# Performance work log

Hardware: AMD Instinct MI355X
Metric: run time of the kernel (lower is better)

The kernel has to match this reference:

```python
import jax, jax.numpy as jnp
import numpy as np
import math

B, E, K, H, NH = 8, 256, 64, 768, 12
HD = H // NH


def setup_inputs() -> dict:
    key = jax.random.key(0)
    ks = jax.random.split(key, 10)
    s = 0.02
    return {
        "q_in": jax.random.normal(ks[0], (B, E, 1, H), jnp.float32),
        "k_in": jax.random.normal(ks[1], (B, E, K, H), jnp.float32),
        "v_in": jax.random.normal(ks[2], (B, E, K, H), jnp.float32),
        "type_score": jax.random.uniform(ks[3], (B, E, 1, 1, K), jnp.float32),
        "Wq": jax.random.normal(ks[4], (H, H), jnp.float32) * s,
        "bq": jnp.zeros((H,), jnp.float32),
        "Wk": jax.random.normal(ks[5], (H, H), jnp.float32) * s,
        "bk": jnp.zeros((H,), jnp.float32),
        "Wv": jax.random.normal(ks[6], (H, H), jnp.float32) * s,
        "bv": jnp.zeros((H,), jnp.float32),
    }


def _heads(x):
    # [B,E,S,H] -> [B,E,nh,S,hd]
    b, e, s, _ = x.shape
    return x.reshape(b, e, s, NH, HD).transpose(0, 1, 3, 2, 4)


def reference(q_in, k_in, v_in, type_score, Wq, bq, Wk, bk, Wv, bv):
    q = _heads(q_in @ Wq.T + bq)   # [B,E,nh,1,hd]
    k = _heads(k_in @ Wk.T + bk)   # [B,E,nh,K,hd]
    v = _heads(v_in @ Wv.T + bv)   # [B,E,nh,K,hd]
    scores = jnp.einsum('behqd,behkd->behqk', q, k) / math.sqrt(HD)
    probs = jax.nn.softmax(scores, axis=-1)
    # post-softmax type reweighting (dropout = identity in eval)
    probs = probs * type_score
    ctx = jnp.einsum('behqk,behkd->behqd', probs, v)   # [B,E,nh,1,hd]
    ctx = ctx.transpose(0, 1, 3, 2, 4).reshape(B, E, 1, H)
    return ctx.squeeze(-2)  # [B,E,H]
```

## Files before the change

kernel.cpp:

```cpp
#include <hip/hip_runtime.h>
#include <stdint.h>

#define Bdim  8
#define Edim  256
#define Kdim  64
#define Hdim  768
#define NHdim 12
#define HDdim 64

typedef __attribute__((ext_vector_type(8))) short short8;
typedef __attribute__((ext_vector_type(4))) float floatx4;
typedef unsigned short ushort_t;
typedef unsigned int u32;

#define GPLANE (2048*768)

__device__ __forceinline__ float bf2f(ushort_t u){
  union { u32 i; float f; } v; v.i = ((u32)u) << 16; return v.f;
}
__device__ __forceinline__ ushort_t f2bf(float f){
  union { float f; u32 i; } v; v.f = f;
  u32 r = v.i + 0x7fffu + ((v.i >> 16) & 1u);
  return (ushort_t)(r >> 16);
}
__device__ __forceinline__ u32 cvtpk(float lo, float hi){
  u32 r;
  asm("v_cvt_pk_bf16_f32 %0, %1, %2" : "=v"(r) : "v"(lo), "v"(hi));
  return r;
}

__device__ __forceinline__ void async_ld16(void* lds, const void* g){
  __builtin_amdgcn_global_load_lds(
      (const __attribute__((address_space(1))) u32*)(uintptr_t)g,
      (__attribute__((address_space(3))) u32*)(u32)(uintptr_t)lds,
      16, 0, 0);
}

__global__ __launch_bounds__(256, 2)
void gemm_proj(const float* __restrict__ A, const ushort_t* __restrict__ W,
               const float* __restrict__ bias, ushort_t* __restrict__ Cout)
{
  __shared__ __align__(16) char smem[34816];
  const int t    = threadIdx.x;
  const int lane = t & 63;
  const int wave = t >> 6;
  const int wm   = wave >> 1, wn = wave & 1;
  const int n0   = blockIdx.x * 128;
  const int m0   = blockIdx.y * 128;

  floatx4 acc[4][4];
#pragma unroll
  for (int i = 0; i < 4; i++)
#pragma unroll
    for (int j = 0; j < 4; j++) acc[i][j] = (floatx4)0.f;

  int am[4], ac[4];
#pragma unroll
  for (int q = 0; q < 4; q++){ int idx = q*256 + t; am[q] = idx >> 3; ac[q] = idx & 7; }

  float4 areg[4];
  const int NT = Hdim / 32;

  char* const smemc = (char*)smem;
  auto Abase = [&](int b){ return smemc + b*16384; };
  auto Wbase = [&](int b){ return smemc + b*16384 + 8192; };

  auto loadA = [&](int kt){
    const float* Ap = A + (size_t)m0*768 + kt*32;
#pragma unroll
    for (int q = 0; q < 4; q++)
      areg[q] = *(const float4*)(Ap + (size_t)am[q]*768 + ac[q]*4);
  };
  auto writeA = [&](int b){
    char* base = Abase(b);
#pragma unroll
    for (int q = 0; q < 4; q++){
      u32 lo = (u32)f2bf(areg[q].x) | ((u32)f2bf(areg[q].y) << 16);
      u32 hi = (u32)f2bf(areg[q].z) | ((u32)f2bf(areg[q].w) << 16);
      int off = am[q]*64 + ((ac[q]*8) ^ ((am[q]&3) << 4));
      u32* p = (u32*)(base + off);
      p[0] = lo; p[1] = hi;
    }
  };
  auto stageW = [&](int kt, int b){
    char* base = Wbase(b);
#pragma unroll
    for (int i = 0; i < 2; i++){
      int s  = i*256 + t;
      int n  = s >> 2, kc = s & 3;
      int kcs = kc ^ (n & 3);
      const ushort_t* g = W + (size_t)(n0 + n)*768 + kt*32 + kcs*8;
      char* ldst = base + (i*256 + wave*64) * 16;
      async_ld16(ldst, g);
    }
  };
  auto compute = [&](int b){
    char* ab = Abase(b);
    char* wb = Wbase(b);
    short8 af[4], bf[4];
#pragma unroll
    for (int mi = 0; mi < 4; mi++){
      int row = wm*64 + mi*16 + (lane & 15);
      int off = row*64 + (((lane >> 4) * 16) ^ ((row & 3) << 4));
      af[mi] = *(const short8*)(ab + off);
    }
#pragma unroll
    for (int ni = 0; ni < 4; ni++){
      int row = wn*64 + ni*16 + (lane & 15);
      int off = row*64 + (((lane >> 4) * 16) ^ ((row & 3) << 4));
      bf[ni] = *(const short8*)(wb + off);
    }
#pragma unroll
    for (int mi = 0; mi < 4; mi++)
#pragma unroll
      for (int ni = 0; ni < 4; ni++)
        acc[mi][ni] = __builtin_amdgcn_mfma_f32_16x16x32_bf16(af[mi], bf[ni], acc[mi][ni], 0, 0, 0);
  };

  int buf = 0;
  loadA(0);
  stageW(0, 0);
  writeA(0);
  asm volatile("s_waitcnt vmcnt(0)" ::: "memory");
  __syncthreads();

  for (int kt = 0; kt < NT; ++kt){
    if (kt + 1 < NT){
      loadA(kt + 1);
      stageW(kt + 1, buf ^ 1);
    }
    compute(buf);
    if (kt + 1 < NT) writeA(buf ^ 1);
    asm volatile("s_waitcnt vmcnt(0)" ::: "memory");
    __syncthreads();
    buf ^= 1;
  }

  float bvv[4];
#pragma unroll
  for (int ni = 0; ni < 4; ni++) bvv[ni] = bias[n0 + wn*64 + ni*16 + (lane & 15)];

  ushort_t* sc = (ushort_t*)smem;
#pragma unroll
  for (int mi = 0; mi < 4; mi++){
    int row0 = wm*64 + mi*16 + ((lane >> 4) << 2);
#pragma unroll
    for (int ni = 0; ni < 4; ni++){
      int col = wn*64 + ni*16 + (lane & 15);
#pragma unroll
      for (int r = 0; r < 4; r++)
        sc[(row0 + r)*136 + col] = f2bf(acc[mi][ni][r] + bvv[ni]);
    }
  }
  __syncthreads();
  int row = t >> 1, seg = t & 1;
  const char* src = smemc + row*272 + seg*128;
  char* dst = (char*)(Cout + (size_t)(m0 + row)*768 + n0 + seg*64);
#pragma unroll
  for (int c = 0; c < 8; c++)
    *(floatx4*)(dst + c*16) = *(const floatx4*)(src + c*16);
}

__global__ __launch_bounds__(256)
void prep(const float* __restrict__ Wq, const float* __restrict__ Wv,
          const float* __restrict__ Wk, ushort_t* __restrict__ Wqb,
          ushort_t* __restrict__ Wvb, ushort_t* __restrict__ WkTb)
{
  __shared__ float tile[32][33];
  const int b = blockIdx.x;
  if (b < 1152){
    const float* src = (b < 576) ? Wq : Wv;
    ushort_t*    dst = (b < 576) ? Wqb : Wvb;
    int bb = (b < 576) ? b : b - 576;
    int i = (bb * 256 + threadIdx.x) * 4;
    float4 v = *(const float4*)(src + i);
    u32* p = (u32*)(dst + i);
    p[0] = (u32)f2bf(v.x) | ((u32)f2bf(v.y) << 16);
    p[1] = (u32)f2bf(v.z) | ((u32)f2bf(v.w) << 16);
  } else {
    int bb = b - 1152;
    int bo = (bb / 24) * 32;
    int bc = (bb % 24) * 32;
    int tx = threadIdx.x & 31, ty = threadIdx.x >> 5;
#pragma unroll
    for (int i = 0; i < 4; i++)
      tile[ty + 8*i][tx] = Wk[(size_t)(bo + ty + 8*i)*768 + bc + tx];
    __syncthreads();
#pragma unroll
    for (int i = 0; i < 4; i++)
      WkTb[(size_t)(bc + ty + 8*i)*768 + bo + tx] = f2bf(tile[tx][ty + 8*i]);
  }
}

__global__ __launch_bounds__(256)
void gemm_g(const ushort_t* __restrict__ qp, const ushort_t* __restrict__ WkT,
            ushort_t* __restrict__ g)
{
  const int h  = blockIdx.z;
  const int n0 = blockIdx.x * 128;
  const int m0 = blockIdx.y * 128;
  const int t = threadIdx.x, lane = t & 63, wave = t >> 6;
  const int wm = wave >> 1, wn = wave & 1;
  const int hl = lane & 15, jr = lane >> 4;

  floatx4 acc[4][4];
#pragma unroll
  for (int i = 0; i < 4; i++)
#pragma unroll
    for (int j = 0; j < 4; j++) acc[i][j] = (floatx4)0.f;

#pragma unroll
  for (int kt = 0; kt < 2; kt++){
    short8 af[4], bf[4];
#pragma unroll
    for (int mi = 0; mi < 4; mi++)
      af[mi] = *(const short8*)(qp + (size_t)(m0 + wm*64 + mi*16 + hl)*768 + h*64 + kt*32 + jr*8);
#pragma unroll
    for (int ni = 0; ni < 4; ni++)
      bf[ni] = *(const short8*)(WkT + (size_t)(n0 + wn*64 + ni*16 + hl)*768 + h*64 + kt*32 + jr*8);
#pragma unroll
    for (int mi = 0; mi < 4; mi++)
#pragma unroll
      for (int ni = 0; ni < 4; ni++)
        acc[mi][ni] = __builtin_amdgcn_mfma_f32_16x16x32_bf16(af[mi], bf[ni], acc[mi][ni], 0, 0, 0);
  }

  ushort_t* gp = g + (size_t)h * GPLANE;
#pragma unroll
  for (int mi = 0; mi < 4; mi++){
#pragma unroll
    for (int ni = 0; ni < 4; ni++){
      int col = n0 + wn*64 + ni*16 + hl;
#pragma unroll
      for (int r = 0; r < 4; r++){
        int row = m0 + wm*64 + mi*16 + jr*4 + r;
        gp[(size_t)row*768 + col] = f2bf(acc[mi][ni][r]);
      }
    }
  }
}

__global__ __launch_bounds__(384)
void attn_main(const float* __restrict__ k_in, const float* __restrict__ v_in,
               const float* __restrict__ tsc, const ushort_t* __restrict__ g,
               ushort_t* __restrict__ Ug, float* __restrict__ ps_g)
{
  const int be = blockIdx.x;
  const int t = threadIdx.x, lane = t & 63, w = t >> 6;
  const int hl = lane & 15, jr = lane >> 4;

  __shared__ float P[12][64];
  __shared__ float redmax[4][16];
  __shared__ float redsum[4][16];

  float s[4], e[4], gm;
  if (w < 4){
    const float* krow = k_in + (size_t)be*Kdim*768 + (size_t)(w*16 + hl)*768;
    const int hq = (hl < 12) ? hl : 0;
    const ushort_t* grow = g + (size_t)hq*GPLANE + (size_t)be*768;

    floatx4 acc = (floatx4)0.f;
#pragma unroll 4
    for (int kt = 0; kt < 24; kt++){
      int c0 = kt*32 + jr*8;
      float4 f0 = *(const float4*)(krow + c0);
      float4 f1 = *(const float4*)(krow + c0 + 4);
      union { short8 s8; u32 wd[4]; } A;
      A.wd[0] = cvtpk(f0.x, f0.y);
      A.wd[1] = cvtpk(f0.z, f0.w);
      A.wd[2] = cvtpk(f1.x, f1.y);
      A.wd[3] = cvtpk(f1.z, f1.w);
      short8 bf = *(const short8*)(grow + c0);
      acc = __builtin_amdgcn_mfma_f32_16x16x32_bf16(A.s8, bf, acc, 0, 0, 0);
    }
#pragma unroll
    for (int r = 0; r < 4; r++) s[r] = acc[r] * 0.125f;

    float wmax = fmaxf(fmaxf(s[0], s[1]), fmaxf(s[2], s[3]));
    wmax = fmaxf(wmax, __shfl_xor(wmax, 16));
    wmax = fmaxf(wmax, __shfl_xor(wmax, 32));
    if (jr == 0) redmax[w][hl] = wmax;
  }
  __syncthreads();
  if (w < 4){
    gm = fmaxf(fmaxf(redmax[0][hl], redmax[1][hl]),
               fmaxf(redmax[2][hl], redmax[3][hl]));
    float es = 0.f;
#pragma unroll
    for (int r = 0; r < 4; r++){ e[r] = __expf(s[r] - gm); es += e[r]; }
    es += __shfl_xor(es, 16);
    es += __shfl_xor(es, 32);
    if (jr == 0) redsum[w][hl] = es;
  }
  __syncthreads();
  if (w < 4 && hl < 12){
    float S = redsum[0][hl] + redsum[1][hl] + redsum[2][hl] + redsum[3][hl];
    float invS = 1.0f / S;
    float4 t4 = *(const float4*)(tsc + be*64 + w*16 + jr*4);
    float4 pv = make_float4(e[0]*invS*t4.x, e[1]*invS*t4.y,
                            e[2]*invS*t4.z, e[3]*invS*t4.w);
    *(float4*)&P[hl][w*16 + jr*4] = pv;
  }
  __syncthreads();

  if (t < 12){
    float sum = 0.f;
#pragma unroll
    for (int jb = 0; jb < 16; jb++){
      float4 p4 = *(const float4*)&P[t][jb*4];
      sum += p4.x + p4.y + p4.z + p4.w;
    }
    ps_g[be*12 + t] = sum;
  }

  const float* vbase = v_in + (size_t)be*Kdim*768 + 2*t;
  float u0[12], u1[12];
#pragma unroll
  for (int h = 0; h < 12; h++){ u0[h] = 0.f; u1[h] = 0.f; }

  for (int jb = 0; jb < 16; jb++){
    float2 v[4];
#pragma unroll
    for (int q = 0; q < 4; q++)
      v[q] = *(const float2*)(vbase + (size_t)(jb*4 + q)*768);
#pragma unroll
    for (int h = 0; h < 12; h++){
      float4 p4 = *(const float4*)&P[h][jb*4];
      u0[h] += p4.x*v[0].x + p4.y*v[1].x + p4.z*v[2].x + p4.w*v[3].x;
      u1[h] += p4.x*v[0].y + p4.y*v[1].y + p4.z*v[2].y + p4.w*v[3].y;
    }
  }

#pragma unroll
  for (int h = 0; h < 12; h++)
    ((u32*)(Ug + (size_t)h*GPLANE + (size_t)be*768))[t] = cvtpk(u0[h], u1[h]);
}

__global__ __launch_bounds__(256)
void out_proj(const ushort_t* __restrict__ Ug, const ushort_t* __restrict__ Wvb,
              const float* __restrict__ bv, const float* __restrict__ ps_g,
              float* __restrict__ out)
{
  const int h  = blockIdx.y;
  const int m0 = blockIdx.x * 128;
  const int t = threadIdx.x, lane = t & 63, wave = t >> 6;
  const int wm = wave >> 1, wn = wave & 1;
  const int hl = lane & 15, jr = lane >> 4;

  const ushort_t* Up = Ug + (size_t)h*GPLANE;

  floatx4 acc[4][2];
#pragma unroll
  for (int i = 0; i < 4; i++){ acc[i][0] = (floatx4)0.f; acc[i][1] = (floatx4)0.f; }

#pragma unroll 4
  for (int kt = 0; kt < 24; kt++){
    short8 af[4], bf[2];
#pragma unroll
    for (int mi = 0; mi < 4; mi++)
      af[mi] = *(const short8*)(Up + (size_t)(m0 + wm*64 + mi*16 + hl)*768 + kt*32 + jr*8);
#pragma unroll
    for (int ni = 0; ni < 2; ni++)
      bf[ni] = *(const short8*)(Wvb + (size_t)(h*64 + wn*32 + ni*16 + hl)*768 + kt*32 + jr*8);
#pragma unroll
    for (int mi = 0; mi < 4; mi++)
#pragma unroll
      for (int ni = 0; ni < 2; ni++)
        acc[mi][ni] = __builtin_amdgcn_mfma_f32_16x16x32_bf16(af[mi], bf[ni], acc[mi][ni], 0, 0, 0);
  }

  float bvo[2];
#pragma unroll
  for (int ni = 0; ni < 2; ni++) bvo[ni] = bv[h*64 + wn*32 + ni*16 + hl];

#pragma unroll
  for (int mi = 0; mi < 4; mi++){
#pragma unroll
    for (int r = 0; r < 4; r++){
      int be = m0 + wm*64 + mi*16 + jr*4 + r;
      float psv = ps_g[be*12 + h];
#pragma unroll
      for (int ni = 0; ni < 2; ni++)
        out[(size_t)be*768 + h*64 + wn*32 + ni*16 + hl] = acc[mi][ni][r] + bvo[ni]*psv;
    }
  }
}

extern "C" void kernel_launch(void* const* d_in, const int* in_sizes, int n_in,
                              void* d_out, int out_size, void* d_ws, size_t ws_size,
                              hipStream_t stream)
{
  const float* q_in = (const float*)d_in[0];
  const float* k_in = (const float*)d_in[1];
  const float* v_in = (const float*)d_in[2];
  const float* tsc  = (const float*)d_in[3];
  const float* Wq   = (const float*)d_in[4];
  const float* bq   = (const float*)d_in[5];
  const float* Wk   = (const float*)d_in[6];
  const float* Wv   = (const float*)d_in[8];
  const float* bv   = (const float*)d_in[9];

  char* ws = (char*)d_ws;
  ushort_t* Wqb  = (ushort_t*)(ws);
  ushort_t* Wvb  = (ushort_t*)(ws + 1179648);
  ushort_t* WkTb = (ushort_t*)(ws + 2359296);
  ushort_t* qp   = (ushort_t*)(ws + 3538944);
  ushort_t* g    = (ushort_t*)(ws + 6684672);
  ushort_t* Ug   = (ushort_t*)(ws + 44433408);
  float*    ps_g = (float*)   (ws + 82182144);

  prep<<<1728, 256, 0, stream>>>(Wq, Wv, Wk, Wqb, Wvb, WkTb);

  gemm_proj<<<dim3(6, 16), 256, 0, stream>>>(q_in, Wqb, bq, qp);

  gemm_g<<<dim3(6, 16, 12), 256, 0, stream>>>(qp, WkTb, g);

  attn_main<<<2048, 384, 0, stream>>>(k_in, v_in, tsc, g, Ug, ps_g);

  out_proj<<<dim3(16, 12), 256, 0, stream>>>(Ug, Wvb, bv, ps_g, (float*)d_out);
}
```

Measured before the change: 268.2 us.

## Split attention into score and value kernels with LDS staging and prefetch

Splits the fused attention kernel into two launches. The first computes scores and softmax with 256 threads, so no waves sit idle, stages the g rows in LDS, and software-prefetches k rows. The second computes the probability-weighted V sums with register double-buffered V loads. The goal is better occupancy and more loads in flight for each phase. The cost is an extra launch and a global round trip for the probabilities.

```diff
diff --git a/kernel.cpp b/kernel.cpp
--- a/kernel.cpp
+++ b/kernel.cpp
@@ -240,67 +240,95 @@
   }
 }
 
-__global__ __launch_bounds__(384)
-void attn_main(const float* __restrict__ k_in, const float* __restrict__ v_in,
-               const float* __restrict__ tsc, const ushort_t* __restrict__ g,
-               ushort_t* __restrict__ Ug, float* __restrict__ ps_g)
+__global__ __launch_bounds__(256)
+void attn_scores(const float* __restrict__ k_in, const float* __restrict__ tsc,
+                 const ushort_t* __restrict__ g, float* __restrict__ probs)
 {
   const int be = blockIdx.x;
   const int t = threadIdx.x, lane = t & 63, w = t >> 6;
   const int hl = lane & 15, jr = lane >> 4;
 
-  __shared__ float P[12][64];
+  __shared__ __align__(16) ushort_t gs[12][776];
   __shared__ float redmax[4][16];
   __shared__ float redsum[4][16];
 
-  float s[4], e[4], gm;
-  if (w < 4){
-    const float* krow = k_in + (size_t)be*Kdim*768 + (size_t)(w*16 + hl)*768;
-    const int hq = (hl < 12) ? hl : 0;
-    const ushort_t* grow = g + (size_t)hq*GPLANE + (size_t)be*768;
-
-    floatx4 acc = (floatx4)0.f;
+  {
+    const ushort_t* gbase = g + (size_t)be*768;
+#pragma unroll
+    for (int c0 = 0; c0 < 1152; c0 += 256){
+      int c = c0 + t;
+      if (c < 1152){
+        int row = c / 96, col = (c % 96) * 8;
+        *(short8*)&gs[row][col] = *(const short8*)(gbase + (size_t)row*GPLANE + col);
+      }
+    }
+  }
+  __syncthreads();
+
+  const float* krow = k_in + (size_t)be*Kdim*768 + (size_t)(w*16 + hl)*768;
+  const int hq = (hl < 12) ? hl : 0;
+
+  floatx4 acc = (floatx4)0.f;
+  float4 f0 = *(const float4*)(krow + jr*8);
+  float4 f1 = *(const float4*)(krow + jr*8 + 4);
 #pragma unroll 4
-    for (int kt = 0; kt < 24; kt++){
-      int c0 = kt*32 + jr*8;
-      float4 f0 = *(const float4*)(krow + c0);
-      float4 f1 = *(const float4*)(krow + c0 + 4);
-      union { short8 s8; u32 wd[4]; } A;
-      A.wd[0] = cvtpk(f0.x, f0.y);
-      A.wd[1] = cvtpk(f0.z, f0.w);
-      A.wd[2] = cvtpk(f1.x, f1.y);
-      A.wd[3] = cvtpk(f1.z, f1.w);
-      short8 bf = *(const short8*)(grow + c0);
-      acc = __builtin_amdgcn_mfma_f32_16x16x32_bf16(A.s8, bf, acc, 0, 0, 0);
-    }
-#pragma unroll
-    for (int r = 0; r < 4; r++) s[r] = acc[r] * 0.125f;
-
-    float wmax = fmaxf(fmaxf(s[0], s[1]), fmaxf(s[2], s[3]));
-    wmax = fmaxf(wmax, __shfl_xor(wmax, 16));
-    wmax = fmaxf(wmax, __shfl_xor(wmax, 32));
-    if (jr == 0) redmax[w][hl] = wmax;
-  }
-  __syncthreads();
-  if (w < 4){
-    gm = fmaxf(fmaxf(redmax[0][hl], redmax[1][hl]),
-               fmaxf(redmax[2][hl], redmax[3][hl]));
-    float es = 0.f;
-#pragma unroll
-    for (int r = 0; r < 4; r++){ e[r] = __expf(s[r] - gm); es += e[r]; }
-    es += __shfl_xor(es, 16);
-    es += __shfl_xor(es, 32);
-    if (jr == 0) redsum[w][hl] = es;
-  }
-  __syncthreads();
-  if (w < 4 && hl < 12){
-    float S = redsum[0][hl] + redsum[1][hl] + redsum[2][hl] + redsum[3][hl];
-    float invS = 1.0f / S;
-    float4 t4 = *(const float4*)(tsc + be*64 + w*16 + jr*4);
+  for (int kt = 0; kt < 24; kt++){
+    float4 nf0, nf1;
+    if (kt + 1 < 24){
+      int c1 = (kt + 1)*32 + jr*8;
+      nf0 = *(const float4*)(krow + c1);
+      nf1 = *(const float4*)(krow + c1 + 4);
+    }
+    union { short8 s8; u32 wd[4]; } A;
+    A.wd[0] = cvtpk(f0.x, f0.y);
+    A.wd[1] = cvtpk(f0.z, f0.w);
+    A.wd[2] = cvtpk(f1.x, f1.y);
+    A.wd[3] = cvtpk(f1.z, f1.w);
+    short8 bf = *(const short8*)&gs[hq][kt*32 + jr*8];
+    acc = __builtin_amdgcn_mfma_f32_16x16x32_bf16(A.s8, bf, acc, 0, 0, 0);
+    f0 = nf0; f1 = nf1;
+  }
+
+  float s[4];
+#pragma unroll
+  for (int r = 0; r < 4; r++) s[r] = acc[r] * 0.125f;
+
+  float wmax = fmaxf(fmaxf(s[0], s[1]), fmaxf(s[2], s[3]));
+  wmax = fmaxf(wmax, __shfl_xor(wmax, 16));
+  wmax = fmaxf(wmax, __shfl_xor(wmax, 32));
+  if (jr == 0) redmax[w][hl] = wmax;
+  __syncthreads();
+  float gm = fmaxf(fmaxf(redmax[0][hl], redmax[1][hl]),
+                   fmaxf(redmax[2][hl], redmax[3][hl]));
+
+  float e[4], es = 0.f;
+#pragma unroll
+  for (int r = 0; r < 4; r++){ e[r] = __expf(s[r] - gm); es += e[r]; }
+  es += __shfl_xor(es, 16);
+  es += __shfl_xor(es, 32);
+  if (jr == 0) redsum[w][hl] = es;
+  __syncthreads();
+  float S = redsum[0][hl] + redsum[1][hl] + redsum[2][hl] + redsum[3][hl];
+  float invS = 1.0f / S;
+
+  float4 t4 = *(const float4*)(tsc + be*64 + w*16 + jr*4);
+  if (hl < 12){
     float4 pv = make_float4(e[0]*invS*t4.x, e[1]*invS*t4.y,
                             e[2]*invS*t4.z, e[3]*invS*t4.w);
-    *(float4*)&P[hl][w*16 + jr*4] = pv;
-  }
+    *(float4*)(probs + (size_t)be*768 + hl*64 + w*16 + jr*4) = pv;
+  }
+}
+
+__global__ __launch_bounds__(384)
+void attn_u(const float* __restrict__ v_in, const float* __restrict__ probs,
+            ushort_t* __restrict__ Ug, float* __restrict__ ps_g)
+{
+  const int be = blockIdx.x;
+  const int t = threadIdx.x;
+
+  __shared__ float P[12][64];
+  ((float*)P)[t]       = probs[(size_t)be*768 + t];
+  ((float*)P)[t + 384] = probs[(size_t)be*768 + t + 384];
   __syncthreads();
 
   if (t < 12){
@@ -318,17 +346,26 @@
 #pragma unroll
   for (int h = 0; h < 12; h++){ u0[h] = 0.f; u1[h] = 0.f; }
 
+  float2 v[4], nv[4];
+#pragma unroll
+  for (int q = 0; q < 4; q++)
+    v[q] = *(const float2*)(vbase + (size_t)q*768);
+
+#pragma unroll 2
   for (int jb = 0; jb < 16; jb++){
-    float2 v[4];
-#pragma unroll
-    for (int q = 0; q < 4; q++)
-      v[q] = *(const float2*)(vbase + (size_t)(jb*4 + q)*768);
+    if (jb + 1 < 16){
+#pragma unroll
+      for (int q = 0; q < 4; q++)
+        nv[q] = *(const float2*)(vbase + (size_t)((jb+1)*4 + q)*768);
+    }
 #pragma unroll
     for (int h = 0; h < 12; h++){
       float4 p4 = *(const float4*)&P[h][jb*4];
       u0[h] += p4.x*v[0].x + p4.y*v[1].x + p4.z*v[2].x + p4.w*v[3].x;
       u1[h] += p4.x*v[0].y + p4.y*v[1].y + p4.z*v[2].y + p4.w*v[3].y;
     }
+#pragma unroll
+    for (int q = 0; q < 4; q++) v[q] = nv[q];
   }
 
 #pragma unroll
@@ -408,6 +445,7 @@
   ushort_t* g    = (ushort_t*)(ws + 6684672);
   ushort_t* Ug   = (ushort_t*)(ws + 44433408);
   float*    ps_g = (float*)   (ws + 82182144);
+  float*    probs= (float*)   (ws + 82280448);
 
   prep<<<1728, 256, 0, stream>>>(Wq, Wv, Wk, Wqb, Wvb, WkTb);
 
@@ -415,7 +453,9 @@
 
   gemm_g<<<dim3(6, 16, 12), 256, 0, stream>>>(qp, WkTb, g);
 
-  attn_main<<<2048, 384, 0, stream>>>(k_in, v_in, tsc, g, Ug, ps_g);
+  attn_scores<<<2048, 256, 0, stream>>>(k_in, tsc, g, probs);
+
+  attn_u<<<2048, 384, 0, stream>>>(v_in, probs, Ug, ps_g);
 
   out_proj<<<dim3(16, 12), 256, 0, stream>>>(Ug, Wvb, bv, ps_g, (float*)d_out);
 }
```

Measured after the change: 263.3 us, median of 2. Within noise of the previous version (-1.9%).
